# Optimization experiments

Hardware: AMD Instinct MI355X
Metric: run time of the kernel (lower is better)

The kernel has to match this reference:

```python
import jax, jax.numpy as jnp
import numpy as np

T, D, H, L = 8192, 1024, 1024, 4


def setup_inputs() -> dict:
    key = jax.random.key(0)
    ks = jax.random.split(key, 1 + 4 * L)
    lim = 1.0 / np.sqrt(H)  # equinox GRUCell uses U(-1/sqrt(hidden), 1/sqrt(hidden))
    inp = {"xs": jax.random.normal(ks[0], (T, D), dtype=jnp.float32)}
    in_sz = D
    for l in range(L):
        k0, k1, k2, k3 = ks[1 + 4 * l: 5 + 4 * l]
        inp[f"Wih{l}"] = jax.random.uniform(k0, (3 * H, in_sz), minval=-lim, maxval=lim, dtype=jnp.float32)
        inp[f"Whh{l}"] = jax.random.uniform(k1, (3 * H, H), minval=-lim, maxval=lim, dtype=jnp.float32)
        inp[f"b{l}"] = jax.random.uniform(k2, (3 * H,), minval=-lim, maxval=lim, dtype=jnp.float32)
        inp[f"bn{l}"] = jax.random.uniform(k3, (H,), minval=-lim, maxval=lim, dtype=jnp.float32)
        in_sz = H
    return inp


def _gru_layer(xs, Wih, Whh, b, bn):
    # Equinox GRUCell math: gates ordered (reset, update, new); h' = n + z*(h - n).
    Hd = Whh.shape[1]
    igates = xs @ Wih.T + b  # (T, 3H): input projections hoisted out of the scan

    def step(h, ig):
        hg = Whh @ h  # (3H,)
        r = jax.nn.sigmoid(ig[:Hd] + hg[:Hd])
        z = jax.nn.sigmoid(ig[Hd:2 * Hd] + hg[Hd:2 * Hd])
        n = jnp.tanh(ig[2 * Hd:] + r * (hg[2 * Hd:] + bn))
        h_new = n + z * (h - n)
        return h_new, h_new

    h0 = jnp.zeros((Hd,), dtype=xs.dtype)
    _, out = jax.lax.scan(step, h0, igates)
    return out  # (T, H)


def reference(xs, Wih0, Whh0, b0, bn0, Wih1, Whh1, b1, bn1,
              Wih2, Whh2, b2, bn2, Wih3, Whh3, b3, bn3):
    for Wih, Whh, b, bn in ((Wih0, Whh0, b0, bn0), (Wih1, Whh1, b1, bn1),
                            (Wih2, Whh2, b2, bn2), (Wih3, Whh3, b3, bn3)):
        xs = _gru_layer(xs, Wih, Whh, b, bn)
    return xs
```

## Files before the change

### kernel.cpp

```cpp
#include <hip/hip_runtime.h>

#define TSTEPS 8192
#define HDIM   1024
#define NLAYER 4
#define NB     256
#define NT     512
#define GB     64
#define EPB    16
#define RING   16

typedef float    f32x4 __attribute__((ext_vector_type(4)));
typedef unsigned u32x4 __attribute__((ext_vector_type(4)));
typedef unsigned long long u64;

struct GruParams {
  const float* xs;
  const float* Wih[NLAYER];
  const float* Whh[NLAYER];
  const float* bias[NLAYER];
  const float* bn[NLAYER];
  float* out;
  int*   ctags;
  u64*   hbp;
  u64*   ringp;
};

__device__ __forceinline__ float sigmoidf_(float x) {
  return 1.0f / (1.0f + __expf(-x));
}
__device__ __forceinline__ float tanhf_(float x) {
  const float e = __expf(2.0f * x);
  return 1.0f - 2.0f / (e + 1.0f);
}
__device__ __forceinline__ float rfl_(float x) {
  return __int_as_float(__builtin_amdgcn_readfirstlane(__float_as_int(x)));
}

__device__ __forceinline__ void poll_stage_row_(const u64* buf, unsigned e,
                                                float* lds, int lane) {
  const u64* p0 = buf + lane * 4;
  u32x4 r0, r1, r2, r3, r4, r5, r6, r7;
  for (;;) {
    asm volatile(
        "global_load_dwordx4 %0, %8, off sc1\n\t"
        "global_load_dwordx4 %1, %9, off sc1\n\t"
        "global_load_dwordx4 %2, %10, off sc1\n\t"
        "global_load_dwordx4 %3, %11, off sc1\n\t"
        "global_load_dwordx4 %4, %12, off sc1\n\t"
        "global_load_dwordx4 %5, %13, off sc1\n\t"
        "global_load_dwordx4 %6, %14, off sc1\n\t"
        "global_load_dwordx4 %7, %15, off sc1\n\t"
        "s_waitcnt vmcnt(0)"
        : "=&v"(r0), "=&v"(r1), "=&v"(r2), "=&v"(r3),
          "=&v"(r4), "=&v"(r5), "=&v"(r6), "=&v"(r7)
        : "v"(p0), "v"(p0 + 2), "v"(p0 + 256), "v"(p0 + 258),
          "v"(p0 + 512), "v"(p0 + 514), "v"(p0 + 768), "v"(p0 + 770)
        : "memory");
    bool ok = (r0.y == e) & (r0.w == e) & (r1.y == e) & (r1.w == e) &
              (r2.y == e) & (r2.w == e) & (r3.y == e) & (r3.w == e) &
              (r4.y == e) & (r4.w == e) & (r5.y == e) & (r5.w == e) &
              (r6.y == e) & (r6.w == e) & (r7.y == e) & (r7.w == e);
    if (__all(ok)) break;
    __builtin_amdgcn_s_sleep(1);
  }
  f32x4 v;
  v.x = __uint_as_float(r0.x); v.y = __uint_as_float(r0.z);
  v.z = __uint_as_float(r1.x); v.w = __uint_as_float(r1.z);
  *reinterpret_cast<f32x4*>(&lds[0 * 256 + lane * 4]) = v;
  v.x = __uint_as_float(r2.x); v.y = __uint_as_float(r2.z);
  v.z = __uint_as_float(r3.x); v.w = __uint_as_float(r3.z);
  *reinterpret_cast<f32x4*>(&lds[1 * 256 + lane * 4]) = v;
  v.x = __uint_as_float(r4.x); v.y = __uint_as_float(r4.z);
  v.z = __uint_as_float(r5.x); v.w = __uint_as_float(r5.z);
  *reinterpret_cast<f32x4*>(&lds[2 * 256 + lane * 4]) = v;
  v.x = __uint_as_float(r6.x); v.y = __uint_as_float(r6.z);
  v.z = __uint_as_float(r7.x); v.w = __uint_as_float(r7.z);
  *reinterpret_cast<f32x4*>(&lds[3 * 256 + lane * 4]) = v;
}

__device__ __forceinline__ void stage_plain_row_(const float* row, float* lds,
                                                 int lane) {
#pragma unroll
  for (int i = 0; i < 4; ++i)
    *reinterpret_cast<f32x4*>(&lds[i * 256 + lane * 4]) =
        *reinterpret_cast<const f32x4*>(row + i * 256 + lane * 4);
}

__global__ __attribute__((amdgpu_flat_work_group_size(NT, NT),
                          amdgpu_waves_per_eu(2, 2)))
void gru_pipe(GruParams p) {
  __shared__ float xst[2][HDIM];
  __shared__ float hst[2][HDIM];
  __shared__ int hflag[2];
  const int tid  = threadIdx.x;
  const int lane = tid & 63;
  const int wave = tid >> 6;
  const int blk  = blockIdx.x;
  const int g    = blk >> 6;
  const int m    = blk & 63;
  const int j0   = m * EPB + wave * 2;

  const float* Wih = p.Wih[g];
  const float* Whh = p.Whh[g];
  f32x4 w4[48];
#pragma unroll
  for (int e = 0; e < 2; ++e) {
#pragma unroll
    for (int dd = 0; dd < 6; ++dd) {
      const float* W = (dd < 3) ? Wih : Whh;
      const int gate = (dd < 3) ? dd : dd - 3;
      const float* src = W + ((size_t)gate * HDIM + (j0 + e)) * HDIM + lane * 4;
#pragma unroll
      for (int i = 0; i < 4; ++i)
        w4[(e * 6 + dd) * 4 + i] = *reinterpret_cast<const f32x4*>(src + i * 256);
    }
  }
  const float bA0 = rfl_(p.bias[g][j0]);
  const float bA1 = rfl_(p.bias[g][HDIM + j0]);
  const float bA2 = rfl_(p.bias[g][2 * HDIM + j0]);
  const float bnA = rfl_(p.bn[g][j0]);
  const float bB0 = rfl_(p.bias[g][j0 + 1]);
  const float bB1 = rfl_(p.bias[g][HDIM + j0 + 1]);
  const float bB2 = rfl_(p.bias[g][2 * HDIM + j0 + 1]);
  const float bnB = rfl_(p.bn[g][j0 + 1]);
  float hregA = 0.f, hregB = 0.f;

  u64* hp = p.hbp + (size_t)g * 2 * HDIM;
  const u64* ring_in  = p.ringp + (size_t)(g - 1) * RING * HDIM;
  u64*       ring_out = p.ringp + (size_t)g * RING * HDIM;

  if (tid == 0) { hflag[0] = -1; hflag[1] = -1; }
  if (wave == 1) {
    if (g == 0)
      stage_plain_row_(p.xs, &xst[0][0], lane);
    else {
      poll_stage_row_(ring_in, 1u, &xst[0][0], lane);
      if (lane == 0)
        __hip_atomic_store(&p.ctags[blk], 1, __ATOMIC_RELAXED,
                           __HIP_MEMORY_SCOPE_AGENT);
    }
  }
  __syncthreads();

  for (int t = 0; t < TSTEPS; ++t) {
    const int par = t & 1;

    float A_ir = 0.f, A_iz = 0.f, A_in = 0.f;
    float B_ir = 0.f, B_iz = 0.f, B_in = 0.f;
#pragma unroll
    for (int i = 0; i < 4; ++i) {
      const f32x4 v = *reinterpret_cast<const f32x4*>(&xst[par][i * 256 + lane * 4]);
#pragma unroll
      for (int q = 0; q < 4; ++q) {
        const float xq = v[q];
        A_ir = fmaf(w4[ 0 + i][q], xq, A_ir);
        A_iz = fmaf(w4[ 4 + i][q], xq, A_iz);
        A_in = fmaf(w4[ 8 + i][q], xq, A_in);
        B_ir = fmaf(w4[24 + i][q], xq, B_ir);
        B_iz = fmaf(w4[28 + i][q], xq, B_iz);
        B_in = fmaf(w4[32 + i][q], xq, B_in);
      }
    }

    if (wave == 0) {
      if (t > 0) {
        poll_stage_row_(hp + (size_t)par * HDIM, (unsigned)t, &hst[par][0], lane);
        asm volatile("s_waitcnt lgkmcnt(0)" ::: "memory");
        if (lane == 0) ((volatile int*)hflag)[par] = t;
      }
    } else if (wave == 1) {
      if (t + 1 < TSTEPS) {
        const int pn = (t + 1) & 1;
        if (g == 0)
          stage_plain_row_(p.xs + (size_t)(t + 1) * HDIM, &xst[pn][0], lane);
        else {
          poll_stage_row_(ring_in + (size_t)((t + 1) & (RING - 1)) * HDIM,
                          (unsigned)(t + 2), &xst[pn][0], lane);
          if (lane == 0)
            __hip_atomic_store(&p.ctags[blk], t + 2, __ATOMIC_RELAXED,
                               __HIP_MEMORY_SCOPE_AGENT);
        }
      }
    } else if (wave == 2) {
      if (g < 3 && t >= RING && (t & 7) == 0) {
        const int bound = t - 8;
        const int* tp = p.ctags + (g + 1) * GB + lane;
        for (;;) {
          const int v = __hip_atomic_load(tp, __ATOMIC_RELAXED,
                                          __HIP_MEMORY_SCOPE_AGENT);
          if (__all(v >= bound)) break;
          __builtin_amdgcn_s_sleep(4);
        }
      }
    }

    float A_hr = 0.f, A_hz = 0.f, A_hn = 0.f;
    float B_hr = 0.f, B_hz = 0.f, B_hn = 0.f;
    if (t > 0) {
      if (wave != 0) {
        while (((volatile int*)hflag)[par] != t) { }
        asm volatile("s_waitcnt lgkmcnt(0)" ::: "memory");
        __builtin_amdgcn_sched_barrier(0);
      }
#pragma unroll
      for (int i = 0; i < 4; ++i) {
        const f32x4 v = *reinterpret_cast<const f32x4*>(&hst[par][i * 256 + lane * 4]);
#pragma unroll
        for (int q = 0; q < 4; ++q) {
          const float hq = v[q];
          A_hr = fmaf(w4[12 + i][q], hq, A_hr);
          A_hz = fmaf(w4[16 + i][q], hq, A_hz);
          A_hn = fmaf(w4[20 + i][q], hq, A_hn);
          B_hr = fmaf(w4[36 + i][q], hq, B_hr);
          B_hz = fmaf(w4[40 + i][q], hq, B_hz);
          B_hn = fmaf(w4[44 + i][q], hq, B_hn);
        }
      }
    }

    float sAr = A_ir + A_hr, sAz = A_iz + A_hz;
    float sBr = B_ir + B_hr, sBz = B_iz + B_hz;
#pragma unroll
    for (int off = 32; off > 0; off >>= 1) {
      sAr  += __shfl_xor(sAr,  off, 64);
      sAz  += __shfl_xor(sAz,  off, 64);
      A_in += __shfl_xor(A_in, off, 64);
      A_hn += __shfl_xor(A_hn, off, 64);
      sBr  += __shfl_xor(sBr,  off, 64);
      sBz  += __shfl_xor(sBz,  off, 64);
      B_in += __shfl_xor(B_in, off, 64);
      B_hn += __shfl_xor(B_hn, off, 64);
    }
    const float rA = sigmoidf_(sAr + bA0);
    const float zA = sigmoidf_(sAz + bA1);
    const float nA = tanhf_(A_in + bA2 + rA * (A_hn + bnA));
    const float hA = nA + zA * (hregA - nA);
    const float rB = sigmoidf_(sBr + bB0);
    const float zB = sigmoidf_(sBz + bB1);
    const float nB = tanhf_(B_in + bB2 + rB * (B_hn + bnB));
    const float hB = nB + zB * (hregB - nB);
    hregA = hA; hregB = hB;

    if (lane == 0) {
      u32x4 pk;
      pk.x = __float_as_uint(hA); pk.y = (unsigned)(t + 1);
      pk.z = __float_as_uint(hB); pk.w = (unsigned)(t + 1);
      u64* hdst = hp + (size_t)((t + 1) & 1) * HDIM + j0;
      asm volatile("global_store_dwordx4 %0, %1, off sc1"
                   :: "v"(hdst), "v"(pk) : "memory");
      if (g < 3) {
        u64* rdst = ring_out + (size_t)(t & (RING - 1)) * HDIM + j0;
        asm volatile("global_store_dwordx4 %0, %1, off sc1"
                     :: "v"(rdst), "v"(pk) : "memory");
      } else {
        const u64 po = ((u64)__float_as_uint(hB) << 32) |
                       (u64)__float_as_uint(hA);
        float* od = p.out + (size_t)t * HDIM + j0;
        asm volatile("global_store_dwordx2 %0, %1, off sc1"
                     :: "v"(od), "v"(po) : "memory");
      }
    }
    __syncthreads();
  }
}

extern "C" void kernel_launch(void* const* d_in, const int* in_sizes, int n_in,
                              void* d_out, int out_size, void* d_ws, size_t ws_size,
                              hipStream_t stream) {
  GruParams p;
  p.xs = (const float*)d_in[0];
  for (int l = 0; l < NLAYER; ++l) {
    p.Wih[l]  = (const float*)d_in[1 + 4 * l];
    p.Whh[l]  = (const float*)d_in[2 + 4 * l];
    p.bias[l] = (const float*)d_in[3 + 4 * l];
    p.bn[l]   = (const float*)d_in[4 + 4 * l];
  }
  char* ws = (char*)d_ws;
  size_t off = 0;
  p.ctags = (int*)(ws + off);
  off += (size_t)NB * sizeof(int);
  off = (off + 255) & ~(size_t)255;
  p.hbp = (u64*)(ws + off);
  const size_t hbp_bytes = (size_t)NLAYER * 2 * HDIM * sizeof(u64);
  off += hbp_bytes;
  p.ringp = (u64*)(ws + off);
  const size_t ring_bytes = (size_t)3 * RING * HDIM * sizeof(u64);
  off += ring_bytes;
  p.out = (float*)d_out;

  (void)hipMemsetAsync(p.ctags, 0, (size_t)NB * sizeof(int), stream);
  (void)hipMemsetAsync(p.hbp, 0, hbp_bytes, stream);
  (void)hipMemsetAsync(p.ringp, 0, ring_bytes, stream);
  gru_pipe<<<dim3(NB), dim3(NT), 0, stream>>>(p);
}
```

Before: 39.03 ms.

## Replace per-step block barrier with LDS counters and deepen input prefetch ring

Removes the __syncthreads at the end of each timestep and replaces it with LDS release/acquire flags and per-slot consumer counters. Waves can now run ahead on the input projection while still waiting on the hidden-state broadcast. Input staging becomes a 4-deep LDS buffer filled by wave 1 once all consumers of a slot have finished. The inter-layer ring doubles to 32 and back-pressure polling happens every 16 steps instead of every 8. The aim is to shrink the serial per-step critical path; the cost is more complex spin-wait logic and a risk of LDS polling contention or ordering bugs.

```diff
diff --git a/kernel.cpp b/kernel.cpp
--- a/kernel.cpp
+++ b/kernel.cpp
@@ -7,7 +7,8 @@
 #define NT     512
 #define GB     64
 #define EPB    16
-#define RING   16
+#define RING   32
+#define XPRE   4
 
 typedef float    f32x4 __attribute__((ext_vector_type(4)));
 typedef unsigned u32x4 __attribute__((ext_vector_type(4)));
@@ -86,12 +87,25 @@
         *reinterpret_cast<const f32x4*>(row + i * 256 + lane * 4);
 }
 
+__device__ __forceinline__ int lds_ld_acq_(const int* p) {
+  return __hip_atomic_load(p, __ATOMIC_ACQUIRE, __HIP_MEMORY_SCOPE_WORKGROUP);
+}
+__device__ __forceinline__ void lds_st_rel_(int* p, int v) {
+  __hip_atomic_store(p, v, __ATOMIC_RELEASE, __HIP_MEMORY_SCOPE_WORKGROUP);
+}
+__device__ __forceinline__ void lds_add_(int* p) {
+  __hip_atomic_fetch_add(p, 1, __ATOMIC_RELEASE, __HIP_MEMORY_SCOPE_WORKGROUP);
+}
+
 __global__ __attribute__((amdgpu_flat_work_group_size(NT, NT),
                           amdgpu_waves_per_eu(2, 2)))
 void gru_pipe(GruParams p) {
-  __shared__ float xst[2][HDIM];
+  __shared__ float xst[XPRE][HDIM];
   __shared__ float hst[2][HDIM];
+  __shared__ int xflag[XPRE];
   __shared__ int hflag[2];
+  __shared__ int xcnt[XPRE];
+  __shared__ int hcnt[2];
   const int tid  = threadIdx.x;
   const int lane = tid & 63;
   const int wave = tid >> 6;
@@ -129,27 +143,45 @@
   const u64* ring_in  = p.ringp + (size_t)(g - 1) * RING * HDIM;
   u64*       ring_out = p.ringp + (size_t)g * RING * HDIM;
 
-  if (tid == 0) { hflag[0] = -1; hflag[1] = -1; }
+  if (tid == 0) {
+    hflag[0] = 0; hflag[1] = -1;
+    hcnt[0] = 0; hcnt[1] = 0;
+#pragma unroll
+    for (int s = 0; s < XPRE; ++s) { xflag[s] = -1; xcnt[s] = 0; }
+  }
+  if (wave == 0) {
+    const f32x4 z4 = {0.f, 0.f, 0.f, 0.f};
+#pragma unroll
+    for (int i = 0; i < 4; ++i)
+      *reinterpret_cast<f32x4*>(&hst[0][i * 256 + lane * 4]) = z4;
+  }
+  __syncthreads();
   if (wave == 1) {
-    if (g == 0)
-      stage_plain_row_(p.xs, &xst[0][0], lane);
-    else {
-      poll_stage_row_(ring_in, 1u, &xst[0][0], lane);
-      if (lane == 0)
-        __hip_atomic_store(&p.ctags[blk], 1, __ATOMIC_RELAXED,
-                           __HIP_MEMORY_SCOPE_AGENT);
-    }
-  }
-  __syncthreads();
+    for (int s = 0; s < XPRE; ++s) {
+      if (g == 0)
+        stage_plain_row_(p.xs + (size_t)s * HDIM, &xst[s][0], lane);
+      else
+        poll_stage_row_(ring_in + (size_t)s * HDIM, (unsigned)(s + 1),
+                        &xst[s][0], lane);
+      asm volatile("s_waitcnt lgkmcnt(0)" ::: "memory");
+      if (lane == 0) lds_st_rel_(&xflag[s], s);
+    }
+    if (g > 0 && lane == 0)
+      __hip_atomic_store(&p.ctags[blk], XPRE, __ATOMIC_RELAXED,
+                         __HIP_MEMORY_SCOPE_AGENT);
+  }
 
   for (int t = 0; t < TSTEPS; ++t) {
+    const int s   = t & (XPRE - 1);
     const int par = t & 1;
 
+    while (lds_ld_acq_(&xflag[s]) < t) { }
+    __builtin_amdgcn_sched_barrier(0);
     float A_ir = 0.f, A_iz = 0.f, A_in = 0.f;
     float B_ir = 0.f, B_iz = 0.f, B_in = 0.f;
 #pragma unroll
     for (int i = 0; i < 4; ++i) {
-      const f32x4 v = *reinterpret_cast<const f32x4*>(&xst[par][i * 256 + lane * 4]);
+      const f32x4 v = *reinterpret_cast<const f32x4*>(&xst[s][i * 256 + lane * 4]);
 #pragma unroll
       for (int q = 0; q < 4; ++q) {
         const float xq = v[q];
@@ -161,62 +193,45 @@
         B_in = fmaf(w4[32 + i][q], xq, B_in);
       }
     }
-
-    if (wave == 0) {
-      if (t > 0) {
-        poll_stage_row_(hp + (size_t)par * HDIM, (unsigned)t, &hst[par][0], lane);
-        asm volatile("s_waitcnt lgkmcnt(0)" ::: "memory");
-        if (lane == 0) ((volatile int*)hflag)[par] = t;
-      }
-    } else if (wave == 1) {
-      if (t + 1 < TSTEPS) {
-        const int pn = (t + 1) & 1;
-        if (g == 0)
-          stage_plain_row_(p.xs + (size_t)(t + 1) * HDIM, &xst[pn][0], lane);
-        else {
-          poll_stage_row_(ring_in + (size_t)((t + 1) & (RING - 1)) * HDIM,
-                          (unsigned)(t + 2), &xst[pn][0], lane);
-          if (lane == 0)
-            __hip_atomic_store(&p.ctags[blk], t + 2, __ATOMIC_RELAXED,
-                               __HIP_MEMORY_SCOPE_AGENT);
-        }
-      }
-    } else if (wave == 2) {
-      if (g < 3 && t >= RING && (t & 7) == 0) {
-        const int bound = t - 8;
-        const int* tp = p.ctags + (g + 1) * GB + lane;
-        for (;;) {
-          const int v = __hip_atomic_load(tp, __ATOMIC_RELAXED,
-                                          __HIP_MEMORY_SCOPE_AGENT);
-          if (__all(v >= bound)) break;
-          __builtin_amdgcn_s_sleep(4);
-        }
-      }
-    }
-
+    if (lane == 0) lds_add_(&xcnt[s]);
+
+    if (wave == 0 && t > 0) {
+      const int need = 8 * (t >> 1);
+      while (lds_ld_acq_(&hcnt[par]) < need) { }
+      poll_stage_row_(hp + (size_t)par * HDIM, (unsigned)t, &hst[par][0], lane);
+      asm volatile("s_waitcnt lgkmcnt(0)" ::: "memory");
+      if (lane == 0) lds_st_rel_(&hflag[par], t);
+    }
+    if (wave == 2 && g < 3 && t >= 16 && (t & 15) == 0) {
+      const int bound = t - 16;
+      const int* tp = p.ctags + (g + 1) * GB + lane;
+      for (;;) {
+        const int v = __hip_atomic_load(tp, __ATOMIC_RELAXED,
+                                        __HIP_MEMORY_SCOPE_AGENT);
+        if (__all(v >= bound)) break;
+        __builtin_amdgcn_s_sleep(4);
+      }
+    }
+
+    while (lds_ld_acq_(&hflag[par]) < t) { }
+    __builtin_amdgcn_sched_barrier(0);
     float A_hr = 0.f, A_hz = 0.f, A_hn = 0.f;
     float B_hr = 0.f, B_hz = 0.f, B_hn = 0.f;
-    if (t > 0) {
-      if (wave != 0) {
-        while (((volatile int*)hflag)[par] != t) { }
-        asm volatile("s_waitcnt lgkmcnt(0)" ::: "memory");
-        __builtin_amdgcn_sched_barrier(0);
-      }
-#pragma unroll
-      for (int i = 0; i < 4; ++i) {
-        const f32x4 v = *reinterpret_cast<const f32x4*>(&hst[par][i * 256 + lane * 4]);
-#pragma unroll
-        for (int q = 0; q < 4; ++q) {
-          const float hq = v[q];
-          A_hr = fmaf(w4[12 + i][q], hq, A_hr);
-          A_hz = fmaf(w4[16 + i][q], hq, A_hz);
-          A_hn = fmaf(w4[20 + i][q], hq, A_hn);
-          B_hr = fmaf(w4[36 + i][q], hq, B_hr);
-          B_hz = fmaf(w4[40 + i][q], hq, B_hz);
-          B_hn = fmaf(w4[44 + i][q], hq, B_hn);
-        }
-      }
-    }
+#pragma unroll
+    for (int i = 0; i < 4; ++i) {
+      const f32x4 v = *reinterpret_cast<const f32x4*>(&hst[par][i * 256 + lane * 4]);
+#pragma unroll
+      for (int q = 0; q < 4; ++q) {
+        const float hq = v[q];
+        A_hr = fmaf(w4[12 + i][q], hq, A_hr);
+        A_hz = fmaf(w4[16 + i][q], hq, A_hz);
+        A_hn = fmaf(w4[20 + i][q], hq, A_hn);
+        B_hr = fmaf(w4[36 + i][q], hq, B_hr);
+        B_hz = fmaf(w4[40 + i][q], hq, B_hz);
+        B_hn = fmaf(w4[44 + i][q], hq, B_hn);
+      }
+    }
+    if (lane == 0) lds_add_(&hcnt[par]);
 
     float sAr = A_ir + A_hr, sAz = A_iz + A_hz;
     float sBr = B_ir + B_hr, sBz = B_iz + B_hz;
@@ -260,7 +275,26 @@
                      :: "v"(od), "v"(po) : "memory");
       }
     }
-    __syncthreads();
+
+    if (wave == 1) {
+      const int tw = t + XPRE;
+      if (tw < TSTEPS) {
+        const int need = 8 * ((t >> 2) + 1);
+        while (lds_ld_acq_(&xcnt[s]) < need) { }
+        if (g == 0)
+          stage_plain_row_(p.xs + (size_t)tw * HDIM, &xst[s][0], lane);
+        else
+          poll_stage_row_(ring_in + (size_t)(tw & (RING - 1)) * HDIM,
+                          (unsigned)(tw + 1), &xst[s][0], lane);
+        asm volatile("s_waitcnt lgkmcnt(0)" ::: "memory");
+        if (lane == 0) {
+          lds_st_rel_(&xflag[s], tw);
+          if (g > 0)
+            __hip_atomic_store(&p.ctags[blk], tw + 1, __ATOMIC_RELAXED,
+                               __HIP_MEMORY_SCOPE_AGENT);
+        }
+      }
+    }
   }
 }
 
```

Result: slower. 42.73 ms (+9.5%).

## Add per-block step tags swept before polling hidden and ring rows

Applied to the files above, without the earlier changes.

Adds a per-block step counter array. Before polling the 8KB hidden-state and ring rows, the waves first sweep these small counters of peer blocks, so that full-row poll traffic does not spin on stale data. The ring depth is doubled and the downstream back-pressure check runs less often with a looser bound. The cost is an extra atomic store per step and an extra flag sweep on the critical recurrence path.

```diff
diff --git a/kernel.cpp b/kernel.cpp
--- a/kernel.cpp
+++ b/kernel.cpp
@@ -7,7 +7,7 @@
 #define NT     512
 #define GB     64
 #define EPB    16
-#define RING   16
+#define RING   32
 
 typedef float    f32x4 __attribute__((ext_vector_type(4)));
 typedef unsigned u32x4 __attribute__((ext_vector_type(4)));
@@ -20,6 +20,7 @@
   const float* bias[NLAYER];
   const float* bn[NLAYER];
   float* out;
+  int*   tags;
   int*   ctags;
   u64*   hbp;
   u64*   ringp;
@@ -34,6 +35,18 @@
 }
 __device__ __forceinline__ float rfl_(float x) {
   return __int_as_float(__builtin_amdgcn_readfirstlane(__float_as_int(x)));
+}
+
+__device__ __forceinline__ void sweep_tags_(const int* tp, int bound,
+                                            int selflane) {
+  const int lane = (int)(threadIdx.x & 63);
+  for (;;) {
+    const int v = __hip_atomic_load(tp, __ATOMIC_RELAXED,
+                                    __HIP_MEMORY_SCOPE_AGENT);
+    const bool ok = (v >= bound) | (lane == selflane);
+    if (__all(ok)) break;
+    __builtin_amdgcn_s_sleep(1);
+  }
 }
 
 __device__ __forceinline__ void poll_stage_row_(const u64* buf, unsigned e,
@@ -128,12 +141,16 @@
   u64* hp = p.hbp + (size_t)g * 2 * HDIM;
   const u64* ring_in  = p.ringp + (size_t)(g - 1) * RING * HDIM;
   u64*       ring_out = p.ringp + (size_t)g * RING * HDIM;
+  const int* owntp = p.tags + g * GB + lane;
+  const int* uptp  = (g > 0) ? (p.tags + (g - 1) * GB + lane) : owntp;
+  const int* dwnp  = (g < 3) ? (p.ctags + (g + 1) * GB + lane) : owntp;
 
   if (tid == 0) { hflag[0] = -1; hflag[1] = -1; }
   if (wave == 1) {
     if (g == 0)
       stage_plain_row_(p.xs, &xst[0][0], lane);
     else {
+      sweep_tags_(uptp, 1, -1);
       poll_stage_row_(ring_in, 1u, &xst[0][0], lane);
       if (lane == 0)
         __hip_atomic_store(&p.ctags[blk], 1, __ATOMIC_RELAXED,
@@ -144,6 +161,10 @@
 
   for (int t = 0; t < TSTEPS; ++t) {
     const int par = t & 1;
+
+    if (tid == 0 && t > 0)
+      __hip_atomic_store(&p.tags[blk], t, __ATOMIC_RELAXED,
+                         __HIP_MEMORY_SCOPE_AGENT);
 
     float A_ir = 0.f, A_iz = 0.f, A_in = 0.f;
     float B_ir = 0.f, B_iz = 0.f, B_in = 0.f;
@@ -164,7 +185,9 @@
 
     if (wave == 0) {
       if (t > 0) {
-        poll_stage_row_(hp + (size_t)par * HDIM, (unsigned)t, &hst[par][0], lane);
+        sweep_tags_(owntp, t, m);
+        poll_stage_row_(hp + (size_t)par * HDIM, (unsigned)t,
+                        &hst[par][0], lane);
         asm volatile("s_waitcnt lgkmcnt(0)" ::: "memory");
         if (lane == 0) ((volatile int*)hflag)[par] = t;
       }
@@ -174,6 +197,7 @@
         if (g == 0)
           stage_plain_row_(p.xs + (size_t)(t + 1) * HDIM, &xst[pn][0], lane);
         else {
+          sweep_tags_(uptp, t + 2, -1);
           poll_stage_row_(ring_in + (size_t)((t + 1) & (RING - 1)) * HDIM,
                           (unsigned)(t + 2), &xst[pn][0], lane);
           if (lane == 0)
@@ -182,9 +206,9 @@
         }
       }
     } else if (wave == 2) {
-      if (g < 3 && t >= RING && (t & 7) == 0) {
-        const int bound = t - 8;
-        const int* tp = p.ctags + (g + 1) * GB + lane;
+      if (g < 3 && t >= 32 && (t & 15) == 0) {
+        const int bound = t - 14;
+        const int* tp = dwnp;
         for (;;) {
           const int v = __hip_atomic_load(tp, __ATOMIC_RELAXED,
                                           __HIP_MEMORY_SCOPE_AGENT);
@@ -262,6 +286,10 @@
     }
     __syncthreads();
   }
+
+  if (tid == 0)
+    __hip_atomic_store(&p.tags[blk], TSTEPS, __ATOMIC_RELAXED,
+                       __HIP_MEMORY_SCOPE_AGENT);
 }
 
 extern "C" void kernel_launch(void* const* d_in, const int* in_sizes, int n_in,
@@ -277,6 +305,8 @@
   }
   char* ws = (char*)d_ws;
   size_t off = 0;
+  p.tags = (int*)(ws + off);
+  off += (size_t)NB * sizeof(int);
   p.ctags = (int*)(ws + off);
   off += (size_t)NB * sizeof(int);
   off = (off + 255) & ~(size_t)255;
@@ -288,7 +318,7 @@
   off += ring_bytes;
   p.out = (float*)d_out;
 
-  (void)hipMemsetAsync(p.ctags, 0, (size_t)NB * sizeof(int), stream);
+  (void)hipMemsetAsync(p.tags, 0, (size_t)2 * NB * sizeof(int), stream);
   (void)hipMemsetAsync(p.hbp, 0, hbp_bytes, stream);
   (void)hipMemsetAsync(p.ringp, 0, ring_bytes, stream);
   gru_pipe<<<dim3(NB), dim3(NT), 0, stream>>>(p);
```

Measured after the change: 55.16 ms. +41.3%, slower.

## Replicate hidden-state and ring buffers so polling blocks read distinct copies

Applied to the files above, without the earlier changes.

Each producer now writes its hidden-state and inter-layer ring entries to 8 replicated copies, and each consumer block polls the copy selected by its block index mod 8. The goal is to spread the spin-polling of 64 blocks across separate cache lines and channels, reducing contention on one hot buffer. The h-state poll is also moved ahead of the input-projection FMAs, and the backpressure check now runs every 4 steps with a different bound. In exchange each lane-0 writer issues 8 times as many stores per step and the workspace grows.

```diff
diff --git a/kernel.cpp b/kernel.cpp
--- a/kernel.cpp
+++ b/kernel.cpp
@@ -8,6 +8,7 @@
 #define GB     64
 #define EPB    16
 #define RING   16
+#define NREP   8
 
 typedef float    f32x4 __attribute__((ext_vector_type(4)));
 typedef unsigned u32x4 __attribute__((ext_vector_type(4)));
@@ -98,6 +99,7 @@
   const int blk  = blockIdx.x;
   const int g    = blk >> 6;
   const int m    = blk & 63;
+  const int rep  = m & (NREP - 1);
   const int j0   = m * EPB + wave * 2;
 
   const float* Wih = p.Wih[g];
@@ -125,16 +127,18 @@
   const float bnB = rfl_(p.bn[g][j0 + 1]);
   float hregA = 0.f, hregB = 0.f;
 
-  u64* hp = p.hbp + (size_t)g * 2 * HDIM;
-  const u64* ring_in  = p.ringp + (size_t)(g - 1) * RING * HDIM;
-  u64*       ring_out = p.ringp + (size_t)g * RING * HDIM;
+  u64* hp = p.hbp + (size_t)g * 2 * NREP * HDIM;
+  const u64* ring_in  = p.ringp + (size_t)(g - 1) * RING * NREP * HDIM;
+  u64*       ring_out = p.ringp + (size_t)g * RING * NREP * HDIM;
+  const int* dwnp = (g < 3) ? (p.ctags + (g + 1) * GB + lane)
+                            : (p.ctags + g * GB + lane);
 
   if (tid == 0) { hflag[0] = -1; hflag[1] = -1; }
   if (wave == 1) {
     if (g == 0)
       stage_plain_row_(p.xs, &xst[0][0], lane);
     else {
-      poll_stage_row_(ring_in, 1u, &xst[0][0], lane);
+      poll_stage_row_(ring_in + (size_t)rep * HDIM, 1u, &xst[0][0], lane);
       if (lane == 0)
         __hip_atomic_store(&p.ctags[blk], 1, __ATOMIC_RELAXED,
                            __HIP_MEMORY_SCOPE_AGENT);
@@ -144,6 +148,15 @@
 
   for (int t = 0; t < TSTEPS; ++t) {
     const int par = t & 1;
+
+    if (wave == 0) {
+      if (t > 0) {
+        poll_stage_row_(hp + ((size_t)par * NREP + rep) * HDIM, (unsigned)t,
+                        &hst[par][0], lane);
+        asm volatile("s_waitcnt lgkmcnt(0)" ::: "memory");
+        if (lane == 0) ((volatile int*)hflag)[par] = t;
+      }
+    }
 
     float A_ir = 0.f, A_iz = 0.f, A_in = 0.f;
     float B_ir = 0.f, B_iz = 0.f, B_in = 0.f;
@@ -162,19 +175,14 @@
       }
     }
 
-    if (wave == 0) {
-      if (t > 0) {
-        poll_stage_row_(hp + (size_t)par * HDIM, (unsigned)t, &hst[par][0], lane);
-        asm volatile("s_waitcnt lgkmcnt(0)" ::: "memory");
-        if (lane == 0) ((volatile int*)hflag)[par] = t;
-      }
-    } else if (wave == 1) {
+    if (wave == 1) {
       if (t + 1 < TSTEPS) {
         const int pn = (t + 1) & 1;
         if (g == 0)
           stage_plain_row_(p.xs + (size_t)(t + 1) * HDIM, &xst[pn][0], lane);
         else {
-          poll_stage_row_(ring_in + (size_t)((t + 1) & (RING - 1)) * HDIM,
+          poll_stage_row_(ring_in +
+                              ((size_t)((t + 1) & (RING - 1)) * NREP + rep) * HDIM,
                           (unsigned)(t + 2), &xst[pn][0], lane);
           if (lane == 0)
             __hip_atomic_store(&p.ctags[blk], t + 2, __ATOMIC_RELAXED,
@@ -182,11 +190,10 @@
         }
       }
     } else if (wave == 2) {
-      if (g < 3 && t >= RING && (t & 7) == 0) {
-        const int bound = t - 8;
-        const int* tp = p.ctags + (g + 1) * GB + lane;
+      if (g < 3 && t >= 16 && (t & 3) == 0) {
+        const int bound = t - 10;
         for (;;) {
-          const int v = __hip_atomic_load(tp, __ATOMIC_RELAXED,
+          const int v = __hip_atomic_load(dwnp, __ATOMIC_RELAXED,
                                           __HIP_MEMORY_SCOPE_AGENT);
           if (__all(v >= bound)) break;
           __builtin_amdgcn_s_sleep(4);
@@ -245,13 +252,17 @@
       u32x4 pk;
       pk.x = __float_as_uint(hA); pk.y = (unsigned)(t + 1);
       pk.z = __float_as_uint(hB); pk.w = (unsigned)(t + 1);
-      u64* hdst = hp + (size_t)((t + 1) & 1) * HDIM + j0;
-      asm volatile("global_store_dwordx4 %0, %1, off sc1"
-                   :: "v"(hdst), "v"(pk) : "memory");
+      u64* hbase = hp + (size_t)((t + 1) & 1) * NREP * HDIM + j0;
+#pragma unroll
+      for (int r2 = 0; r2 < NREP; ++r2)
+        asm volatile("global_store_dwordx4 %0, %1, off sc1"
+                     :: "v"(hbase + (size_t)r2 * HDIM), "v"(pk) : "memory");
       if (g < 3) {
-        u64* rdst = ring_out + (size_t)(t & (RING - 1)) * HDIM + j0;
-        asm volatile("global_store_dwordx4 %0, %1, off sc1"
-                     :: "v"(rdst), "v"(pk) : "memory");
+        u64* rbase = ring_out + (size_t)(t & (RING - 1)) * NREP * HDIM + j0;
+#pragma unroll
+        for (int r2 = 0; r2 < NREP; ++r2)
+          asm volatile("global_store_dwordx4 %0, %1, off sc1"
+                       :: "v"(rbase + (size_t)r2 * HDIM), "v"(pk) : "memory");
       } else {
         const u64 po = ((u64)__float_as_uint(hB) << 32) |
                        (u64)__float_as_uint(hA);
@@ -281,10 +292,10 @@
   off += (size_t)NB * sizeof(int);
   off = (off + 255) & ~(size_t)255;
   p.hbp = (u64*)(ws + off);
-  const size_t hbp_bytes = (size_t)NLAYER * 2 * HDIM * sizeof(u64);
+  const size_t hbp_bytes = (size_t)NLAYER * 2 * NREP * HDIM * sizeof(u64);
   off += hbp_bytes;
   p.ringp = (u64*)(ws + off);
-  const size_t ring_bytes = (size_t)3 * RING * HDIM * sizeof(u64);
+  const size_t ring_bytes = (size_t)3 * RING * NREP * HDIM * sizeof(u64);
   off += ring_bytes;
   p.out = (float*)d_out;
 
```

Result: faster. 38.06 ms (-2.5%).
